# Kernel optimization log

Hardware: AMD Instinct MI355X
Metric: run time of the kernel (lower is better)

The kernel has to match this reference:

```python
import jax, jax.numpy as jnp
import numpy as np

N = 100000   # nodes
E = 3200000  # edges (avg degree 32)
D = 128      # in_channels
H = 128      # hidden_channels
A, S, ETH = 3, 2, 3  # head output dims


def _w(k, o, i):
    return jax.random.normal(k, (o, i), dtype=jnp.float32) / np.sqrt(i).astype(np.float32)


def setup_inputs() -> dict:
    key = jax.random.key(0)
    ks = jax.random.split(key, 20)
    x = jax.random.normal(ks[0], (N, D), dtype=jnp.float32)
    edge_index = jax.random.randint(ks[1], (2, E), 0, N, dtype=jnp.int64)
    inp = {"x": x, "edge_index": edge_index}
    # SAGEConv params: Wl applied to mean-aggregated neighbors, Wr to root, plus bias
    dims = [("1", D, H), ("2", H, H), ("3", H, H), ("a", H, A), ("s", H, S), ("e", H, ETH)]
    ki = 2
    for tag, i, o in dims:
        inp[f"W{tag}l"] = _w(ks[ki], o, i); ki += 1
        inp[f"W{tag}r"] = _w(ks[ki], o, i); ki += 1
        inp[f"b{tag}"] = jnp.zeros((o,), dtype=jnp.float32)
    return inp


def _sage(x, src, dst, inv_deg, Wl, Wr, b):
    # mean aggregation of source features onto destination nodes, then linear
    agg = jax.ops.segment_sum(x[src], dst, num_segments=N) * inv_deg  # [N, d]
    return agg @ Wl.T + x @ Wr.T + b


def reference(x, edge_index,
              W1l, W1r, b1, W2l, W2r, b2, W3l, W3r, b3,
              Wal, War, ba, Wsl, Wsr, bs, Wel, Wer, be):
    src, dst = edge_index[0], edge_index[1]
    deg = jax.ops.segment_sum(jnp.ones((E,), jnp.float32), dst, num_segments=N)
    inv_deg = (1.0 / jnp.maximum(deg, 1.0))[:, None]  # [N,1]
    h = jax.nn.relu(_sage(x, src, dst, inv_deg, W1l, W1r, b1))
    h = jax.nn.relu(_sage(h, src, dst, inv_deg, W2l, W2r, b2))
    h = jax.nn.relu(_sage(h, src, dst, inv_deg, W3l, W3r, b3))
    age_out = _sage(h, src, dst, inv_deg, Wal, War, ba)
    sex_out = _sage(h, src, dst, inv_deg, Wsl, Wsr, bs)
    eth_out = _sage(h, src, dst, inv_deg, Wel, Wer, be)
    return (age_out, sex_out, eth_out)
```

## Files before the change

### kernel.cpp

```cpp
#include <hip/hip_runtime.h>

#define TPB 256
#define NB1 256
#define NBUCK 512

using half4_t = __attribute__((ext_vector_type(4))) _Float16;
using half8_t = __attribute__((ext_vector_type(8))) _Float16;
using f32x4 = __attribute__((ext_vector_type(4))) float;


__global__ __launch_bounds__(256) void hist1_k(const int* __restrict__ ei,
                                               int* __restrict__ hist, int E, int stripe) {
  __shared__ int h[NBUCK];
  for (int i = threadIdx.x; i < NBUCK; i += 256) h[i] = 0;
  __syncthreads();
  int b0 = blockIdx.x * stripe;
  int b1 = min(b0 + stripe, E);
  for (int e = b0 + threadIdx.x; e < b1; e += 256) atomicAdd(&h[ei[E + e] >> 8], 1);
  __syncthreads();
  for (int i = threadIdx.x; i < NBUCK; i += 256) hist[i * NB1 + blockIdx.x] = h[i];
}

__global__ void scan1_k(const int* __restrict__ src, int* __restrict__ out,
                        int* __restrict__ chunk, int n) {
  __shared__ int sh[TPB];
  int i = blockIdx.x * TPB + threadIdx.x;
  int v = (i < n) ? src[i] : 0;
  sh[threadIdx.x] = v;
  __syncthreads();
  for (int off = 1; off < TPB; off <<= 1) {
    int t = (threadIdx.x >= off) ? sh[threadIdx.x - off] : 0;
    __syncthreads();
    sh[threadIdx.x] += t;
    __syncthreads();
  }
  if (i < n) out[i] = sh[threadIdx.x] - v;
  if (threadIdx.x == TPB - 1) chunk[blockIdx.x] = sh[TPB - 1];
}

__global__ void scan2_k(int* __restrict__ chunk, int nb) {
  __shared__ int sh[512];
  int v = (threadIdx.x < nb) ? chunk[threadIdx.x] : 0;
  sh[threadIdx.x] = v;
  __syncthreads();
  for (int off = 1; off < 512; off <<= 1) {
    int t = (threadIdx.x >= off) ? sh[threadIdx.x - off] : 0;
    __syncthreads();
    sh[threadIdx.x] += t;
    __syncthreads();
  }
  if (threadIdx.x < nb) chunk[threadIdx.x] = sh[threadIdx.x] - v;
}

__global__ void scan3_k(int* __restrict__ out, const int* __restrict__ chunk, int n) {
  int i = blockIdx.x * TPB + threadIdx.x;
  if (i < n) out[i] += chunk[blockIdx.x];
}

__global__ __launch_bounds__(256) void scatter1_k(const int* __restrict__ ei,
                                                  const int* __restrict__ base,
                                                  unsigned* __restrict__ ebuf, int E,
                                                  int stripe) {
  __shared__ int cur[NBUCK];
  for (int i = threadIdx.x; i < NBUCK; i += 256) cur[i] = base[i * NB1 + blockIdx.x];
  __syncthreads();
  int b0 = blockIdx.x * stripe;
  int b1 = min(b0 + stripe, E);
  for (int e = b0 + threadIdx.x; e < b1; e += 256) {
    int s = ei[e];
    int d = ei[E + e];
    int p = atomicAdd(&cur[d >> 8], 1);
    ebuf[p] = (unsigned)s | ((unsigned)(d & 255) << 24);
  }
}

__global__ __launch_bounds__(256) void build_k(const unsigned* __restrict__ ebuf,
                                               const int* __restrict__ base,
                                               int* __restrict__ row_start,
                                               int* __restrict__ deg,
                                               float* __restrict__ invd,
                                               int* __restrict__ csr, int N, int E) {
  __shared__ int h[256];
  __shared__ int excl[256];
  __shared__ int bse[2];
  int b = blockIdx.x;
  int t = threadIdx.x;
  if (t == 0) {
    bse[0] = base[b * NB1];
    bse[1] = (b + 1 < NBUCK) ? base[(b + 1) * NB1] : E;
  }
  h[t] = 0;
  __syncthreads();
  int bs = bse[0], be = bse[1];
  for (int e = bs + t; e < be; e += 256) atomicAdd(&h[ebuf[e] >> 24], 1);
  __syncthreads();
  int v = h[t];
  excl[t] = v;
  __syncthreads();
  for (int off = 1; off < 256; off <<= 1) {
    int tv = (t >= off) ? excl[t - off] : 0;
    __syncthreads();
    excl[t] += tv;
    __syncthreads();
  }
  int ex = excl[t] - v;
  int node = b * 256 + t;
  if (node < N) {
    row_start[node] = bs + ex;
    deg[node] = v;
    invd[node] = 1.0f / fmaxf((float)v, 1.0f);
  }
  h[t] = bs + ex;
  __syncthreads();
  for (int e = bs + t; e < be; e += 256) {
    unsigned p = ebuf[e];
    int pos = atomicAdd(&h[p >> 24], 1);
    csr[pos] = (int)(p & 0xFFFFFFu);
  }
}


__global__ void f2h_k(const float* __restrict__ in, _Float16* __restrict__ out, int n4) {
  int i = blockIdx.x * TPB + threadIdx.x;
  if (i < n4) {
    float4 v = ((const float4*)in)[i];
    half4_t o;
    o.x = (_Float16)v.x; o.y = (_Float16)v.y; o.z = (_Float16)v.z; o.w = (_Float16)v.w;
    ((half4_t*)out)[i] = o;
  }
}

__global__ void w6_k(const float* __restrict__ w0, const float* __restrict__ w1,
                     const float* __restrict__ w2, const float* __restrict__ w3,
                     const float* __restrict__ w4, const float* __restrict__ w5,
                     _Float16* __restrict__ out) {
  int t = blockIdx.x * TPB + threadIdx.x;
  if (t >= 6 * 4096) return;
  int which = t >> 12, i = t & 4095;
  const float* src = which == 0 ? w0 : which == 1 ? w1 : which == 2 ? w2
                   : which == 3 ? w3 : which == 4 ? w4 : w5;
  float4 v = ((const float4*)src)[i];
  half4_t o;
  o.x = (_Float16)v.x; o.y = (_Float16)v.y; o.z = (_Float16)v.z; o.w = (_Float16)v.w;
  ((half4_t*)out)[(size_t)which * 4096 + i] = o;
}


__global__ void pack_head_k(const float* __restrict__ Wal, const float* __restrict__ War,
                            const float* __restrict__ ba, const float* __restrict__ Wsl,
                            const float* __restrict__ Wsr, const float* __restrict__ bsx,
                            const float* __restrict__ Wel, const float* __restrict__ Wer,
                            const float* __restrict__ be, _Float16* __restrict__ Wcat,
                            float* __restrict__ bcat) {
  int t = blockIdx.x * TPB + threadIdx.x;
  float v = 0.f;
  bool ok = t < 2048;
  if (t < 384) v = Wal[t];
  else if (t < 640) v = Wsl[t - 384];
  else if (t < 1024) v = Wel[t - 640];
  else if (t < 1408) v = War[t - 1024];
  else if (t < 1664) v = Wsr[t - 1408];
  else if (t < 2048) v = Wer[t - 1664];
  if (ok) Wcat[t] = (_Float16)v;
  if (t < 16) {
    float b = 0.f;
    if (t >= 8 && t < 11) b = ba[t - 8];
    else if (t >= 11 && t < 13) b = bsx[t - 11];
    else if (t >= 13) b = be[t - 13];
    bcat[t] = b;
  }
}


__global__ __launch_bounds__(256) void fused_sage_k(
    const _Float16* __restrict__ hin, const _Float16* __restrict__ Wh,
    const float* __restrict__ bias, const int* __restrict__ csr,
    const int* __restrict__ row_start, const int* __restrict__ deg,
    const float* __restrict__ invd, _Float16* __restrict__ hout,
    const _Float16* __restrict__ Wcat, const float* __restrict__ bcat,
    float* __restrict__ head_out, int n, int mode) {
  __shared__ _Float16 At[16][144];
  int wave = threadIdx.x >> 6;
  int lane = threadIdx.x & 63;
  int g = lane >> 4;
  int l = lane & 15;
  int ms = blockIdx.x * 16;

  const _Float16* gbase = hin + (l << 3);
  int nb = ms + wave * 4;
  int rs[4], dg[4];
#pragma unroll
  for (int i = 0; i < 4; ++i) {
    int nd = nb + i;
    bool ok = nd < n;
    rs[i] = ok ? row_start[nd] : 0;
    dg[i] = ok ? deg[nd] : 0;
  }
  int nid[4];
  if (dg[0] >= 16) {
#pragma unroll
    for (int p = 0; p < 4; ++p) nid[p] = csr[rs[0] + 4 * p + g];
  }
  for (int i = 0; i < 4; ++i) {
    int s = rs[i], c = dg[i];
    float a0 = 0.f, a1 = 0.f, a2 = 0.f, a3 = 0.f;
    float a4 = 0.f, a5 = 0.f, a6 = 0.f, a7 = 0.f;
    int j = 0;
    if (c >= 16) {
      int id[4];
#pragma unroll
      for (int p = 0; p < 4; ++p) id[p] = nid[p];
      while (true) {
        half8_t v[4];
#pragma unroll
        for (int p = 0; p < 4; ++p) v[p] = *(const half8_t*)&gbase[(size_t)id[p] * 128];
        j += 16;
        bool more = (j + 16 <= c);
        if (more) {
#pragma unroll
          for (int p = 0; p < 4; ++p) id[p] = csr[s + j + 4 * p + g];
        }
#pragma unroll
        for (int p = 0; p < 4; ++p) {
          a0 += (float)v[p][0]; a1 += (float)v[p][1];
          a2 += (float)v[p][2]; a3 += (float)v[p][3];
          a4 += (float)v[p][4]; a5 += (float)v[p][5];
          a6 += (float)v[p][6]; a7 += (float)v[p][7];
        }
        if (!more) break;
      }
    }
    if (i < 3 && dg[i + 1] >= 16) {
#pragma unroll
      for (int p = 0; p < 4; ++p) nid[p] = csr[rs[i + 1] + 4 * p + g];
    }
    if (j < c) {
      int cm1 = c - 1;
#pragma unroll
      for (int p = 0; p < 4; ++p) {
        int e = j + 4 * p + g;
        float m = (e < c) ? 1.f : 0.f;
        int id = csr[s + min(e, cm1)];
        half8_t v = *(const half8_t*)&gbase[(size_t)id * 128];
        a0 = fmaf(m, (float)v[0], a0); a1 = fmaf(m, (float)v[1], a1);
        a2 = fmaf(m, (float)v[2], a2); a3 = fmaf(m, (float)v[3], a3);
        a4 = fmaf(m, (float)v[4], a4); a5 = fmaf(m, (float)v[5], a5);
        a6 = fmaf(m, (float)v[6], a6); a7 = fmaf(m, (float)v[7], a7);
      }
    }
    a0 += __shfl_xor(a0, 16); a1 += __shfl_xor(a1, 16);
    a2 += __shfl_xor(a2, 16); a3 += __shfl_xor(a3, 16);
    a4 += __shfl_xor(a4, 16); a5 += __shfl_xor(a5, 16);
    a6 += __shfl_xor(a6, 16); a7 += __shfl_xor(a7, 16);
    a0 += __shfl_xor(a0, 32); a1 += __shfl_xor(a1, 32);
    a2 += __shfl_xor(a2, 32); a3 += __shfl_xor(a3, 32);
    a4 += __shfl_xor(a4, 32); a5 += __shfl_xor(a5, 32);
    a6 += __shfl_xor(a6, 32); a7 += __shfl_xor(a7, 32);
    if (g == 0) {
      int node = nb + i;
      float w = (node < n) ? invd[node] : 0.f;
      half8_t r;
      r[0] = (_Float16)(a0 * w); r[1] = (_Float16)(a1 * w);
      r[2] = (_Float16)(a2 * w); r[3] = (_Float16)(a3 * w);
      r[4] = (_Float16)(a4 * w); r[5] = (_Float16)(a5 * w);
      r[6] = (_Float16)(a6 * w); r[7] = (_Float16)(a7 * w);
      *(half8_t*)&At[wave * 4 + i][l << 3] = r;
    }
  }
  __syncthreads();

  int arow = ms + l;
  bool valid = arow < n;
  f32x4 acc[2];
  acc[0] = (f32x4){0.f, 0.f, 0.f, 0.f};
  acc[1] = (f32x4){0.f, 0.f, 0.f, 0.f};

#pragma unroll
  for (int kb = 0; kb < 128; kb += 32) {
    half8_t af = *(const half8_t*)&At[l][kb + g * 8];
#pragma unroll
    for (int ct = 0; ct < 2; ++ct) {
      int ocol = wave * 32 + ct * 16 + l;
      half8_t bf = *(const half8_t*)&Wh[(size_t)ocol * 128 + kb + g * 8];
      acc[ct] = __builtin_amdgcn_mfma_f32_16x16x32_f16(af, bf, acc[ct], 0, 0, 0);
    }
  }
  {
    const _Float16* W2 = Wh + 16384;
    size_t abase = (size_t)arow * 128 + g * 8;
#pragma unroll
    for (int kb = 0; kb < 128; kb += 32) {
      half8_t af;
      if (valid) {
        af = *(const half8_t*)&hin[abase + kb];
      } else {
#pragma unroll
        for (int jj = 0; jj < 8; ++jj) af[jj] = (_Float16)0;
      }
#pragma unroll
      for (int ct = 0; ct < 2; ++ct) {
        int ocol = wave * 32 + ct * 16 + l;
        half8_t bf = *(const half8_t*)&W2[(size_t)ocol * 128 + kb + g * 8];
        acc[ct] = __builtin_amdgcn_mfma_f32_16x16x32_f16(af, bf, acc[ct], 0, 0, 0);
      }
    }
  }

  if (mode == 0) {
#pragma unroll
    for (int ct = 0; ct < 2; ++ct) {
      int col = wave * 32 + ct * 16 + l;
      float bcol = bias[col];
#pragma unroll
      for (int r = 0; r < 4; ++r) {
        int row = ms + g * 4 + r;
        if (row < n) {
          float v = fmaxf(acc[ct][r] + bcol, 0.f);
          hout[(size_t)row * 128 + col] = (_Float16)v;
        }
      }
    }
  } else {
    __syncthreads();
#pragma unroll
    for (int ct = 0; ct < 2; ++ct) {
      int col = wave * 32 + ct * 16 + l;
      float bcol = bias[col];
#pragma unroll
      for (int r = 0; r < 4; ++r) {
        float v = fmaxf(acc[ct][r] + bcol, 0.f);
        At[g * 4 + r][col] = (_Float16)v;
      }
    }
    __syncthreads();
    if (wave == 0) {
      f32x4 ah = (f32x4){0.f, 0.f, 0.f, 0.f};
#pragma unroll
      for (int kb = 0; kb < 128; kb += 32) {
        half8_t af = *(const half8_t*)&At[l][kb + g * 8];
        half8_t bf = *(const half8_t*)&Wcat[(size_t)l * 128 + kb + g * 8];
        ah = __builtin_amdgcn_mfma_f32_16x16x32_f16(af, bf, ah, 0, 0, 0);
      }
      float bcol = bcat[l];
#pragma unroll
      for (int r = 0; r < 4; ++r) {
        int row = ms + g * 4 + r;
        if (row < n) head_out[(size_t)row * 16 + l] = ah[r] + bcol;
      }
    }
  }
}


__global__ void agg8_k(const float* __restrict__ hlr, const int* __restrict__ csr,
                       const int* __restrict__ row_start, const int* __restrict__ deg,
                       const float* __restrict__ invd, float* __restrict__ out, int n) {
  int node = (blockIdx.x << 2) + (threadIdx.x >> 6);
  if (node >= n) return;
  int lane = threadIdx.x & 63;
  int c2 = lane & 3;
  int g = lane >> 2;
  int s = row_start[node], cnt = deg[node];
  float ax = 0.f, ay = 0.f;
  int j = 0;
  for (; j + 32 <= cnt; j += 32) {
#pragma unroll
    for (int p = 0; p < 2; ++p) {
      int id = csr[s + j + 16 * p + g];
      float2 v = *(const float2*)&hlr[(size_t)id * 16 + 2 * c2];
      ax += v.x;
      ay += v.y;
    }
  }
  if (j < cnt) {
    int cm1 = cnt - 1;
#pragma unroll
    for (int p = 0; p < 2; ++p) {
      int e = j + 16 * p + g;
      float m = (e < cnt) ? 1.f : 0.f;
      int id = csr[s + min(e, cm1)];
      float2 v = *(const float2*)&hlr[(size_t)id * 16 + 2 * c2];
      ax = fmaf(m, v.x, ax);
      ay = fmaf(m, v.y, ay);
    }
  }
  ax += __shfl_xor(ax, 4);  ay += __shfl_xor(ay, 4);
  ax += __shfl_xor(ax, 8);  ay += __shfl_xor(ay, 8);
  ax += __shfl_xor(ax, 16); ay += __shfl_xor(ay, 16);
  ax += __shfl_xor(ax, 32); ay += __shfl_xor(ay, 32);
  if (g == 0) {
    float w = invd[node];
    float r0 = ax * w + hlr[(size_t)node * 16 + 8 + 2 * c2];
    float r1 = ay * w + hlr[(size_t)node * 16 + 8 + 2 * c2 + 1];
    float rr[2] = {r0, r1};
#pragma unroll
    for (int q = 0; q < 2; ++q) {
      int f = 2 * c2 + q;
      float r = rr[q];
      if (f < 3) out[(size_t)node * 3 + f] = r;
      else if (f < 5) out[(size_t)3 * n + (size_t)node * 2 + (f - 3)] = r;
      else out[(size_t)5 * n + (size_t)node * 3 + (f - 5)] = r;
    }
  }
}


extern "C" void kernel_launch(void* const* d_in, const int* in_sizes, int n_in,
                              void* d_out, int out_size, void* d_ws, size_t ws_size,
                              hipStream_t stream) {
  const float* x = (const float*)d_in[0];
  const int* ei = (const int*)d_in[1];
  const float* W1l = (const float*)d_in[2];
  const float* W1r = (const float*)d_in[3];
  const float* b1 = (const float*)d_in[4];
  const float* W2l = (const float*)d_in[5];
  const float* W2r = (const float*)d_in[6];
  const float* b2 = (const float*)d_in[7];
  const float* W3l = (const float*)d_in[8];
  const float* W3r = (const float*)d_in[9];
  const float* b3 = (const float*)d_in[10];
  const float* Wal = (const float*)d_in[11];
  const float* War = (const float*)d_in[12];
  const float* ba = (const float*)d_in[13];
  const float* Wsl = (const float*)d_in[14];
  const float* Wsr = (const float*)d_in[15];
  const float* bsx = (const float*)d_in[16];
  const float* Wel = (const float*)d_in[17];
  const float* Wer = (const float*)d_in[18];
  const float* be = (const float*)d_in[19];

  int N = in_sizes[0] / 128;
  int E = in_sizes[1] / 2;
  int NBKT = (N + 255) >> 8;

  char* w = (char*)d_ws;
  auto alloc = [&](size_t b) {
    char* p = w;
    w += (b + 255) & ~(size_t)255;
    return p;
  };
  int* deg = (int*)alloc((size_t)N * 4);
  int* row_start = (int*)alloc((size_t)N * 4);
  float* invd = (float*)alloc((size_t)N * 4);
  int* hist = (int*)alloc((size_t)NBUCK * NB1 * 4);
  int* chunk = (int*)alloc(512 * 4);
  int* csr = (int*)alloc((size_t)E * 4);
  size_t xh_bytes = (size_t)N * 128 * 2;
  size_t ebuf_bytes = (size_t)E * 4;
  char* region = (char*)alloc(xh_bytes > ebuf_bytes ? xh_bytes : ebuf_bytes);
  unsigned* ebuf = (unsigned*)region;
  _Float16* xh = (_Float16*)region;
  _Float16* hA = (_Float16*)alloc((size_t)N * 128 * 2);
  _Float16* hB = (_Float16*)alloc((size_t)N * 128 * 2);
  _Float16* wh = (_Float16*)alloc((size_t)6 * 16384 * 2);
  _Float16* Wcat = (_Float16*)alloc(2048 * 2);
  float* bcat = (float*)alloc(16 * 4);
  float* head_lr = (float*)alloc((size_t)N * 16 * 4);

  int stripe = (((E + NB1 - 1) / NB1) + 255) & ~255;
  int nscan = NBUCK * NB1;
  int nbScan = (nscan + TPB - 1) / TPB;
  int nbNode = (N + 3) / 4;
  int nbM = (N + 15) / 16;
  int nbC = (N * 32 + TPB - 1) / TPB;

  hist1_k<<<NB1, 256, 0, stream>>>(ei, hist, E, stripe);
  scan1_k<<<nbScan, TPB, 0, stream>>>(hist, hist, chunk, nscan);
  scan2_k<<<1, 512, 0, stream>>>(chunk, nbScan);
  scan3_k<<<nbScan, TPB, 0, stream>>>(hist, chunk, nscan);
  scatter1_k<<<NB1, 256, 0, stream>>>(ei, hist, ebuf, E, stripe);
  build_k<<<NBKT, 256, 0, stream>>>(ebuf, hist, row_start, deg, invd, csr, N, E);

  f2h_k<<<nbC, TPB, 0, stream>>>(x, xh, N * 32);
  w6_k<<<96, TPB, 0, stream>>>(W1l, W1r, W2l, W2r, W3l, W3r, wh);
  pack_head_k<<<8, TPB, 0, stream>>>(Wal, War, ba, Wsl, Wsr, bsx, Wel, Wer, be, Wcat, bcat);

  fused_sage_k<<<nbM, TPB, 0, stream>>>(xh, wh + 0 * 16384, b1, csr, row_start, deg,
                                        invd, hA, nullptr, nullptr, nullptr, N, 0);
  fused_sage_k<<<nbM, TPB, 0, stream>>>(hA, wh + 2 * 16384, b2, csr, row_start, deg,
                                        invd, hB, nullptr, nullptr, nullptr, N, 0);
  fused_sage_k<<<nbM, TPB, 0, stream>>>(hB, wh + 4 * 16384, b3, csr, row_start, deg,
                                        invd, nullptr, Wcat, bcat, head_lr, N, 1);
  agg8_k<<<nbNode, TPB, 0, stream>>>(head_lr, csr, row_start, deg, invd, (float*)d_out, N);
}
```

Measured before the change: 688.4 us.

## Make fused SAGE layer wave-independent, removing block-wide barriers

Each wave now owns its own 4-node tile and private LDS buffers, then computes all 128 output columns with MFMA using only 4 of the 16 A rows (replicated via l&3). This drops every __syncthreads, so waves no longer wait on the slowest gather in the block. Outputs are staged in LDS so hout is written as coalesced half8 rows, and the head GEMM runs per wave. In exchange, each wave does four times the MFMA work and weight loads per node, since 12 of the 16 rows are redundant.

```diff
diff --git a/kernel.cpp b/kernel.cpp
--- a/kernel.cpp
+++ b/kernel.cpp
@@ -179,19 +179,23 @@
     const float* __restrict__ invd, _Float16* __restrict__ hout,
     const _Float16* __restrict__ Wcat, const float* __restrict__ bcat,
     float* __restrict__ head_out, int n, int mode) {
-  __shared__ _Float16 At[16][144];
+  __shared__ _Float16 At[4][4][144];
+  __shared__ _Float16 Ot4[4][4][144];
   int wave = threadIdx.x >> 6;
   int lane = threadIdx.x & 63;
   int g = lane >> 4;
   int l = lane & 15;
-  int ms = blockIdx.x * 16;
+  _Float16(*A)[144] = At[wave];
+  _Float16(*Ot)[144] = Ot4[wave];
+
+  int tb = (blockIdx.x * 4 + wave) * 4;
+  if (tb >= n) return;
 
   const _Float16* gbase = hin + (l << 3);
-  int nb = ms + wave * 4;
   int rs[4], dg[4];
 #pragma unroll
   for (int i = 0; i < 4; ++i) {
-    int nd = nb + i;
+    int nd = tb + i;
     bool ok = nd < n;
     rs[i] = ok ? row_start[nd] : 0;
     dg[i] = ok ? deg[nd] : 0;
@@ -257,95 +261,84 @@
     a4 += __shfl_xor(a4, 32); a5 += __shfl_xor(a5, 32);
     a6 += __shfl_xor(a6, 32); a7 += __shfl_xor(a7, 32);
     if (g == 0) {
-      int node = nb + i;
+      int node = tb + i;
       float w = (node < n) ? invd[node] : 0.f;
       half8_t r;
       r[0] = (_Float16)(a0 * w); r[1] = (_Float16)(a1 * w);
       r[2] = (_Float16)(a2 * w); r[3] = (_Float16)(a3 * w);
       r[4] = (_Float16)(a4 * w); r[5] = (_Float16)(a5 * w);
       r[6] = (_Float16)(a6 * w); r[7] = (_Float16)(a7 * w);
-      *(half8_t*)&At[wave * 4 + i][l << 3] = r;
-    }
-  }
-  __syncthreads();
-
-  int arow = ms + l;
-  bool valid = arow < n;
-  f32x4 acc[2];
-  acc[0] = (f32x4){0.f, 0.f, 0.f, 0.f};
-  acc[1] = (f32x4){0.f, 0.f, 0.f, 0.f};
-
-#pragma unroll
-  for (int kb = 0; kb < 128; kb += 32) {
-    half8_t af = *(const half8_t*)&At[l][kb + g * 8];
-#pragma unroll
-    for (int ct = 0; ct < 2; ++ct) {
-      int ocol = wave * 32 + ct * 16 + l;
-      half8_t bf = *(const half8_t*)&Wh[(size_t)ocol * 128 + kb + g * 8];
-      acc[ct] = __builtin_amdgcn_mfma_f32_16x16x32_f16(af, bf, acc[ct], 0, 0, 0);
-    }
-  }
-  {
-    const _Float16* W2 = Wh + 16384;
-    size_t abase = (size_t)arow * 128 + g * 8;
+      *(half8_t*)&A[i][l << 3] = r;
+    }
+  }
+
+  const _Float16* W2 = Wh + 16384;
+  int rrow = tb + (l & 3);
+  bool rv = rrow < n;
+  size_t rbase = (size_t)rrow * 128 + g * 8;
+#pragma unroll
+  for (int ch = 0; ch < 2; ++ch) {
+    f32x4 acc[4];
+#pragma unroll
+    for (int ct = 0; ct < 4; ++ct) acc[ct] = (f32x4){0.f, 0.f, 0.f, 0.f};
+#pragma unroll
+    for (int kb = 0; kb < 128; kb += 32) {
+      half8_t af = *(const half8_t*)&A[l & 3][kb + g * 8];
+#pragma unroll
+      for (int ct = 0; ct < 4; ++ct) {
+        int col = ch * 64 + ct * 16 + l;
+        half8_t bf = *(const half8_t*)&Wh[(size_t)col * 128 + kb + g * 8];
+        acc[ct] = __builtin_amdgcn_mfma_f32_16x16x32_f16(af, bf, acc[ct], 0, 0, 0);
+      }
+    }
 #pragma unroll
     for (int kb = 0; kb < 128; kb += 32) {
       half8_t af;
-      if (valid) {
-        af = *(const half8_t*)&hin[abase + kb];
+      if (rv) {
+        af = *(const half8_t*)&hin[rbase + kb];
       } else {
 #pragma unroll
         for (int jj = 0; jj < 8; ++jj) af[jj] = (_Float16)0;
       }
 #pragma unroll
-      for (int ct = 0; ct < 2; ++ct) {
-        int ocol = wave * 32 + ct * 16 + l;
-        half8_t bf = *(const half8_t*)&W2[(size_t)ocol * 128 + kb + g * 8];
+      for (int ct = 0; ct < 4; ++ct) {
+        int col = ch * 64 + ct * 16 + l;
+        half8_t bf = *(const half8_t*)&W2[(size_t)col * 128 + kb + g * 8];
         acc[ct] = __builtin_amdgcn_mfma_f32_16x16x32_f16(af, bf, acc[ct], 0, 0, 0);
       }
     }
+    if (g == 0) {
+#pragma unroll
+      for (int ct = 0; ct < 4; ++ct) {
+        int col = ch * 64 + ct * 16 + l;
+        float bc = bias[col];
+#pragma unroll
+        for (int r = 0; r < 4; ++r) {
+          Ot[r][col] = (_Float16)fmaxf(acc[ct][r] + bc, 0.f);
+        }
+      }
+    }
   }
 
   if (mode == 0) {
-#pragma unroll
-    for (int ct = 0; ct < 2; ++ct) {
-      int col = wave * 32 + ct * 16 + l;
-      float bcol = bias[col];
+    int rr = lane >> 4, j = lane & 15;
+    int orow = tb + rr;
+    if (orow < n)
+      *(half8_t*)&hout[(size_t)orow * 128 + j * 8] = *(const half8_t*)&Ot[rr][j * 8];
+  } else {
+    f32x4 ah = (f32x4){0.f, 0.f, 0.f, 0.f};
+#pragma unroll
+    for (int kb = 0; kb < 128; kb += 32) {
+      half8_t af = *(const half8_t*)&Ot[l & 3][kb + g * 8];
+      half8_t bf = *(const half8_t*)&Wcat[(size_t)l * 128 + kb + g * 8];
+      ah = __builtin_amdgcn_mfma_f32_16x16x32_f16(af, bf, ah, 0, 0, 0);
+    }
+    if (g == 0) {
+      float bc = bcat[l];
 #pragma unroll
       for (int r = 0; r < 4; ++r) {
-        int row = ms + g * 4 + r;
-        if (row < n) {
-          float v = fmaxf(acc[ct][r] + bcol, 0.f);
-          hout[(size_t)row * 128 + col] = (_Float16)v;
-        }
-      }
-    }
-  } else {
-    __syncthreads();
-#pragma unroll
-    for (int ct = 0; ct < 2; ++ct) {
-      int col = wave * 32 + ct * 16 + l;
-      float bcol = bias[col];
-#pragma unroll
-      for (int r = 0; r < 4; ++r) {
-        float v = fmaxf(acc[ct][r] + bcol, 0.f);
-        At[g * 4 + r][col] = (_Float16)v;
-      }
-    }
-    __syncthreads();
-    if (wave == 0) {
-      f32x4 ah = (f32x4){0.f, 0.f, 0.f, 0.f};
-#pragma unroll
-      for (int kb = 0; kb < 128; kb += 32) {
-        half8_t af = *(const half8_t*)&At[l][kb + g * 8];
-        half8_t bf = *(const half8_t*)&Wcat[(size_t)l * 128 + kb + g * 8];
-        ah = __builtin_amdgcn_mfma_f32_16x16x32_f16(af, bf, ah, 0, 0, 0);
-      }
-      float bcol = bcat[l];
-#pragma unroll
-      for (int r = 0; r < 4; ++r) {
-        int row = ms + g * 4 + r;
-        if (row < n) head_out[(size_t)row * 16 + l] = ah[r] + bcol;
+        int orow = tb + r;
+        if (orow < n) head_out[(size_t)orow * 16 + l] = ah[r] + bc;
       }
     }
   }
```

Result: slower. 1.123 ms (+63.2%).

## Use persistent atomic tile scheduling, merge prep kernels, split head buffers

Applied to the files above, without the earlier changes.

The three SAGE layer kernels now run a fixed grid of 2048 persistent blocks. Each block pulls 16-node tiles from a global atomic counter until none remain, instead of launching one block per tile. This aims to balance degree-dependent work and cut block-launch overhead, at the cost of one atomic and one barrier per tile. The three small conversion and packing kernels are merged into one prep kernel that also zeroes the tile counters, saving launches. The head output is split into separate 8-wide gather and root buffers, so the final aggregation gathers denser 32-byte rows.

```diff
diff --git a/kernel.cpp b/kernel.cpp
--- a/kernel.cpp
+++ b/kernel.cpp
@@ -120,48 +120,43 @@
 }
 
 
-__global__ void f2h_k(const float* __restrict__ in, _Float16* __restrict__ out, int n4) {
-  int i = blockIdx.x * TPB + threadIdx.x;
-  if (i < n4) {
-    float4 v = ((const float4*)in)[i];
+__global__ void prep_k(const float* __restrict__ x, _Float16* __restrict__ xh, int n4,
+                       const float* __restrict__ w0, const float* __restrict__ w1,
+                       const float* __restrict__ w2, const float* __restrict__ w3,
+                       const float* __restrict__ w4, const float* __restrict__ w5,
+                       _Float16* __restrict__ wh,
+                       const float* __restrict__ Wal, const float* __restrict__ War,
+                       const float* __restrict__ ba, const float* __restrict__ Wsl,
+                       const float* __restrict__ Wsr, const float* __restrict__ bsx,
+                       const float* __restrict__ Wel, const float* __restrict__ Wer,
+                       const float* __restrict__ be, _Float16* __restrict__ Wcat,
+                       float* __restrict__ bcat, int* __restrict__ ctrs) {
+  int t = blockIdx.x * TPB + threadIdx.x;
+  if (t < n4) {
+    float4 v = ((const float4*)x)[t];
     half4_t o;
     o.x = (_Float16)v.x; o.y = (_Float16)v.y; o.z = (_Float16)v.z; o.w = (_Float16)v.w;
-    ((half4_t*)out)[i] = o;
-  }
-}
-
-__global__ void w6_k(const float* __restrict__ w0, const float* __restrict__ w1,
-                     const float* __restrict__ w2, const float* __restrict__ w3,
-                     const float* __restrict__ w4, const float* __restrict__ w5,
-                     _Float16* __restrict__ out) {
-  int t = blockIdx.x * TPB + threadIdx.x;
-  if (t >= 6 * 4096) return;
-  int which = t >> 12, i = t & 4095;
-  const float* src = which == 0 ? w0 : which == 1 ? w1 : which == 2 ? w2
-                   : which == 3 ? w3 : which == 4 ? w4 : w5;
-  float4 v = ((const float4*)src)[i];
-  half4_t o;
-  o.x = (_Float16)v.x; o.y = (_Float16)v.y; o.z = (_Float16)v.z; o.w = (_Float16)v.w;
-  ((half4_t*)out)[(size_t)which * 4096 + i] = o;
-}
-
-
-__global__ void pack_head_k(const float* __restrict__ Wal, const float* __restrict__ War,
-                            const float* __restrict__ ba, const float* __restrict__ Wsl,
-                            const float* __restrict__ Wsr, const float* __restrict__ bsx,
-                            const float* __restrict__ Wel, const float* __restrict__ Wer,
-                            const float* __restrict__ be, _Float16* __restrict__ Wcat,
-                            float* __restrict__ bcat) {
-  int t = blockIdx.x * TPB + threadIdx.x;
-  float v = 0.f;
-  bool ok = t < 2048;
-  if (t < 384) v = Wal[t];
-  else if (t < 640) v = Wsl[t - 384];
-  else if (t < 1024) v = Wel[t - 640];
-  else if (t < 1408) v = War[t - 1024];
-  else if (t < 1664) v = Wsr[t - 1408];
-  else if (t < 2048) v = Wer[t - 1664];
-  if (ok) Wcat[t] = (_Float16)v;
+    ((half4_t*)xh)[t] = o;
+  }
+  if (t < 6 * 4096) {
+    int which = t >> 12, i = t & 4095;
+    const float* src = which == 0 ? w0 : which == 1 ? w1 : which == 2 ? w2
+                     : which == 3 ? w3 : which == 4 ? w4 : w5;
+    float4 v = ((const float4*)src)[i];
+    half4_t o;
+    o.x = (_Float16)v.x; o.y = (_Float16)v.y; o.z = (_Float16)v.z; o.w = (_Float16)v.w;
+    ((half4_t*)wh)[(size_t)which * 4096 + i] = o;
+  }
+  if (t < 2048) {
+    float v = 0.f;
+    if (t < 384) v = Wal[t];
+    else if (t < 640) v = Wsl[t - 384];
+    else if (t < 1024) v = Wel[t - 640];
+    else if (t < 1408) v = War[t - 1024];
+    else if (t < 1664) v = Wsr[t - 1408];
+    else v = Wer[t - 1664];
+    Wcat[t] = (_Float16)v;
+  }
   if (t < 16) {
     float b = 0.f;
     if (t >= 8 && t < 11) b = ba[t - 8];
@@ -169,6 +164,7 @@
     else if (t >= 13) b = be[t - 13];
     bcat[t] = b;
   }
+  if (t < 4) ctrs[t] = 0;
 }
 
 
@@ -178,183 +174,197 @@
     const int* __restrict__ row_start, const int* __restrict__ deg,
     const float* __restrict__ invd, _Float16* __restrict__ hout,
     const _Float16* __restrict__ Wcat, const float* __restrict__ bcat,
-    float* __restrict__ head_out, int n, int mode) {
+    float* __restrict__ head_g, float* __restrict__ head_r,
+    int* __restrict__ ctr, int ntiles, int n, int mode) {
   __shared__ _Float16 At[16][144];
+  __shared__ int tile_s;
   int wave = threadIdx.x >> 6;
   int lane = threadIdx.x & 63;
   int g = lane >> 4;
   int l = lane & 15;
-  int ms = blockIdx.x * 16;
-
   const _Float16* gbase = hin + (l << 3);
-  int nb = ms + wave * 4;
-  int rs[4], dg[4];
-#pragma unroll
-  for (int i = 0; i < 4; ++i) {
-    int nd = nb + i;
-    bool ok = nd < n;
-    rs[i] = ok ? row_start[nd] : 0;
-    dg[i] = ok ? deg[nd] : 0;
-  }
-  int nid[4];
-  if (dg[0] >= 16) {
-#pragma unroll
-    for (int p = 0; p < 4; ++p) nid[p] = csr[rs[0] + 4 * p + g];
-  }
-  for (int i = 0; i < 4; ++i) {
-    int s = rs[i], c = dg[i];
-    float a0 = 0.f, a1 = 0.f, a2 = 0.f, a3 = 0.f;
-    float a4 = 0.f, a5 = 0.f, a6 = 0.f, a7 = 0.f;
-    int j = 0;
-    if (c >= 16) {
-      int id[4];
-#pragma unroll
-      for (int p = 0; p < 4; ++p) id[p] = nid[p];
-      while (true) {
-        half8_t v[4];
-#pragma unroll
-        for (int p = 0; p < 4; ++p) v[p] = *(const half8_t*)&gbase[(size_t)id[p] * 128];
-        j += 16;
-        bool more = (j + 16 <= c);
-        if (more) {
-#pragma unroll
-          for (int p = 0; p < 4; ++p) id[p] = csr[s + j + 4 * p + g];
-        }
+  const _Float16* W2 = Wh + 16384;
+
+  for (;;) {
+    if (threadIdx.x == 0) tile_s = atomicAdd(ctr, 1);
+    __syncthreads();
+    int tile = tile_s;
+    if (tile >= ntiles) break;
+    int ms = tile * 16;
+
+    int nb = ms + wave * 4;
+    int rs[4], dg[4];
+#pragma unroll
+    for (int i = 0; i < 4; ++i) {
+      int nd = nb + i;
+      bool ok = nd < n;
+      rs[i] = ok ? row_start[nd] : 0;
+      dg[i] = ok ? deg[nd] : 0;
+    }
+    int nid[4];
+    if (dg[0] >= 16) {
+#pragma unroll
+      for (int p = 0; p < 4; ++p) nid[p] = csr[rs[0] + 4 * p + g];
+    }
+    for (int i = 0; i < 4; ++i) {
+      int s = rs[i], c = dg[i];
+      float a0 = 0.f, a1 = 0.f, a2 = 0.f, a3 = 0.f;
+      float a4 = 0.f, a5 = 0.f, a6 = 0.f, a7 = 0.f;
+      int j = 0;
+      if (c >= 16) {
+        int id[4];
+#pragma unroll
+        for (int p = 0; p < 4; ++p) id[p] = nid[p];
+        while (true) {
+          half8_t v[4];
+#pragma unroll
+          for (int p = 0; p < 4; ++p) v[p] = *(const half8_t*)&gbase[(size_t)id[p] * 128];
+          j += 16;
+          bool more = (j + 16 <= c);
+          if (more) {
+#pragma unroll
+            for (int p = 0; p < 4; ++p) id[p] = csr[s + j + 4 * p + g];
+          }
+#pragma unroll
+          for (int p = 0; p < 4; ++p) {
+            a0 += (float)v[p][0]; a1 += (float)v[p][1];
+            a2 += (float)v[p][2]; a3 += (float)v[p][3];
+            a4 += (float)v[p][4]; a5 += (float)v[p][5];
+            a6 += (float)v[p][6]; a7 += (float)v[p][7];
+          }
+          if (!more) break;
+        }
+      }
+      if (i < 3 && dg[i + 1] >= 16) {
+#pragma unroll
+        for (int p = 0; p < 4; ++p) nid[p] = csr[rs[i + 1] + 4 * p + g];
+      }
+      if (j < c) {
+        int cm1 = c - 1;
 #pragma unroll
         for (int p = 0; p < 4; ++p) {
-          a0 += (float)v[p][0]; a1 += (float)v[p][1];
-          a2 += (float)v[p][2]; a3 += (float)v[p][3];
-          a4 += (float)v[p][4]; a5 += (float)v[p][5];
-          a6 += (float)v[p][6]; a7 += (float)v[p][7];
-        }
-        if (!more) break;
-      }
-    }
-    if (i < 3 && dg[i + 1] >= 16) {
-#pragma unroll
-      for (int p = 0; p < 4; ++p) nid[p] = csr[rs[i + 1] + 4 * p + g];
-    }
-    if (j < c) {
-      int cm1 = c - 1;
-#pragma unroll
-      for (int p = 0; p < 4; ++p) {
-        int e = j + 4 * p + g;
-        float m = (e < c) ? 1.f : 0.f;
-        int id = csr[s + min(e, cm1)];
-        half8_t v = *(const half8_t*)&gbase[(size_t)id * 128];
-        a0 = fmaf(m, (float)v[0], a0); a1 = fmaf(m, (float)v[1], a1);
-        a2 = fmaf(m, (float)v[2], a2); a3 = fmaf(m, (float)v[3], a3);
-        a4 = fmaf(m, (float)v[4], a4); a5 = fmaf(m, (float)v[5], a5);
-        a6 = fmaf(m, (float)v[6], a6); a7 = fmaf(m, (float)v[7], a7);
-      }
-    }
-    a0 += __shfl_xor(a0, 16); a1 += __shfl_xor(a1, 16);
-    a2 += __shfl_xor(a2, 16); a3 += __shfl_xor(a3, 16);
-    a4 += __shfl_xor(a4, 16); a5 += __shfl_xor(a5, 16);
-    a6 += __shfl_xor(a6, 16); a7 += __shfl_xor(a7, 16);
-    a0 += __shfl_xor(a0, 32); a1 += __shfl_xor(a1, 32);
-    a2 += __shfl_xor(a2, 32); a3 += __shfl_xor(a3, 32);
-    a4 += __shfl_xor(a4, 32); a5 += __shfl_xor(a5, 32);
-    a6 += __shfl_xor(a6, 32); a7 += __shfl_xor(a7, 32);
-    if (g == 0) {
-      int node = nb + i;
-      float w = (node < n) ? invd[node] : 0.f;
-      half8_t r;
-      r[0] = (_Float16)(a0 * w); r[1] = (_Float16)(a1 * w);
-      r[2] = (_Float16)(a2 * w); r[3] = (_Float16)(a3 * w);
-      r[4] = (_Float16)(a4 * w); r[5] = (_Float16)(a5 * w);
-      r[6] = (_Float16)(a6 * w); r[7] = (_Float16)(a7 * w);
-      *(half8_t*)&At[wave * 4 + i][l << 3] = r;
-    }
-  }
-  __syncthreads();
-
-  int arow = ms + l;
-  bool valid = arow < n;
-  f32x4 acc[2];
-  acc[0] = (f32x4){0.f, 0.f, 0.f, 0.f};
-  acc[1] = (f32x4){0.f, 0.f, 0.f, 0.f};
-
-#pragma unroll
-  for (int kb = 0; kb < 128; kb += 32) {
-    half8_t af = *(const half8_t*)&At[l][kb + g * 8];
-#pragma unroll
-    for (int ct = 0; ct < 2; ++ct) {
-      int ocol = wave * 32 + ct * 16 + l;
-      half8_t bf = *(const half8_t*)&Wh[(size_t)ocol * 128 + kb + g * 8];
-      acc[ct] = __builtin_amdgcn_mfma_f32_16x16x32_f16(af, bf, acc[ct], 0, 0, 0);
-    }
-  }
-  {
-    const _Float16* W2 = Wh + 16384;
-    size_t abase = (size_t)arow * 128 + g * 8;
+          int e = j + 4 * p + g;
+          float m = (e < c) ? 1.f : 0.f;
+          int id = csr[s + min(e, cm1)];
+          half8_t v = *(const half8_t*)&gbase[(size_t)id * 128];
+          a0 = fmaf(m, (float)v[0], a0); a1 = fmaf(m, (float)v[1], a1);
+          a2 = fmaf(m, (float)v[2], a2); a3 = fmaf(m, (float)v[3], a3);
+          a4 = fmaf(m, (float)v[4], a4); a5 = fmaf(m, (float)v[5], a5);
+          a6 = fmaf(m, (float)v[6], a6); a7 = fmaf(m, (float)v[7], a7);
+        }
+      }
+      a0 += __shfl_xor(a0, 16); a1 += __shfl_xor(a1, 16);
+      a2 += __shfl_xor(a2, 16); a3 += __shfl_xor(a3, 16);
+      a4 += __shfl_xor(a4, 16); a5 += __shfl_xor(a5, 16);
+      a6 += __shfl_xor(a6, 16); a7 += __shfl_xor(a7, 16);
+      a0 += __shfl_xor(a0, 32); a1 += __shfl_xor(a1, 32);
+      a2 += __shfl_xor(a2, 32); a3 += __shfl_xor(a3, 32);
+      a4 += __shfl_xor(a4, 32); a5 += __shfl_xor(a5, 32);
+      a6 += __shfl_xor(a6, 32); a7 += __shfl_xor(a7, 32);
+      if (g == 0) {
+        int node = nb + i;
+        float w = (node < n) ? invd[node] : 0.f;
+        half8_t r;
+        r[0] = (_Float16)(a0 * w); r[1] = (_Float16)(a1 * w);
+        r[2] = (_Float16)(a2 * w); r[3] = (_Float16)(a3 * w);
+        r[4] = (_Float16)(a4 * w); r[5] = (_Float16)(a5 * w);
+        r[6] = (_Float16)(a6 * w); r[7] = (_Float16)(a7 * w);
+        *(half8_t*)&At[wave * 4 + i][l << 3] = r;
+      }
+    }
+    __syncthreads();
+
+    int arow = ms + l;
+    bool valid = arow < n;
+    f32x4 acc[2];
+    acc[0] = (f32x4){0.f, 0.f, 0.f, 0.f};
+    acc[1] = (f32x4){0.f, 0.f, 0.f, 0.f};
+
 #pragma unroll
     for (int kb = 0; kb < 128; kb += 32) {
-      half8_t af;
-      if (valid) {
-        af = *(const half8_t*)&hin[abase + kb];
-      } else {
-#pragma unroll
-        for (int jj = 0; jj < 8; ++jj) af[jj] = (_Float16)0;
-      }
+      half8_t af = *(const half8_t*)&At[l][kb + g * 8];
 #pragma unroll
       for (int ct = 0; ct < 2; ++ct) {
         int ocol = wave * 32 + ct * 16 + l;
-        half8_t bf = *(const half8_t*)&W2[(size_t)ocol * 128 + kb + g * 8];
+        half8_t bf = *(const half8_t*)&Wh[(size_t)ocol * 128 + kb + g * 8];
         acc[ct] = __builtin_amdgcn_mfma_f32_16x16x32_f16(af, bf, acc[ct], 0, 0, 0);
       }
     }
-  }
-
-  if (mode == 0) {
-#pragma unroll
-    for (int ct = 0; ct < 2; ++ct) {
-      int col = wave * 32 + ct * 16 + l;
-      float bcol = bias[col];
-#pragma unroll
-      for (int r = 0; r < 4; ++r) {
-        int row = ms + g * 4 + r;
-        if (row < n) {
+    {
+      size_t abase = (size_t)arow * 128 + g * 8;
+#pragma unroll
+      for (int kb = 0; kb < 128; kb += 32) {
+        half8_t af;
+        if (valid) {
+          af = *(const half8_t*)&hin[abase + kb];
+        } else {
+#pragma unroll
+          for (int jj = 0; jj < 8; ++jj) af[jj] = (_Float16)0;
+        }
+#pragma unroll
+        for (int ct = 0; ct < 2; ++ct) {
+          int ocol = wave * 32 + ct * 16 + l;
+          half8_t bf = *(const half8_t*)&W2[(size_t)ocol * 128 + kb + g * 8];
+          acc[ct] = __builtin_amdgcn_mfma_f32_16x16x32_f16(af, bf, acc[ct], 0, 0, 0);
+        }
+      }
+    }
+
+    if (mode == 0) {
+#pragma unroll
+      for (int ct = 0; ct < 2; ++ct) {
+        int col = wave * 32 + ct * 16 + l;
+        float bcol = bias[col];
+#pragma unroll
+        for (int r = 0; r < 4; ++r) {
+          int row = ms + g * 4 + r;
+          if (row < n) {
+            float v = fmaxf(acc[ct][r] + bcol, 0.f);
+            hout[(size_t)row * 128 + col] = (_Float16)v;
+          }
+        }
+      }
+    } else {
+      __syncthreads();
+#pragma unroll
+      for (int ct = 0; ct < 2; ++ct) {
+        int col = wave * 32 + ct * 16 + l;
+        float bcol = bias[col];
+#pragma unroll
+        for (int r = 0; r < 4; ++r) {
           float v = fmaxf(acc[ct][r] + bcol, 0.f);
-          hout[(size_t)row * 128 + col] = (_Float16)v;
-        }
-      }
-    }
-  } else {
-    __syncthreads();
-#pragma unroll
-    for (int ct = 0; ct < 2; ++ct) {
-      int col = wave * 32 + ct * 16 + l;
-      float bcol = bias[col];
-#pragma unroll
-      for (int r = 0; r < 4; ++r) {
-        float v = fmaxf(acc[ct][r] + bcol, 0.f);
-        At[g * 4 + r][col] = (_Float16)v;
-      }
-    }
-    __syncthreads();
-    if (wave == 0) {
-      f32x4 ah = (f32x4){0.f, 0.f, 0.f, 0.f};
-#pragma unroll
-      for (int kb = 0; kb < 128; kb += 32) {
-        half8_t af = *(const half8_t*)&At[l][kb + g * 8];
-        half8_t bf = *(const half8_t*)&Wcat[(size_t)l * 128 + kb + g * 8];
-        ah = __builtin_amdgcn_mfma_f32_16x16x32_f16(af, bf, ah, 0, 0, 0);
-      }
-      float bcol = bcat[l];
-#pragma unroll
-      for (int r = 0; r < 4; ++r) {
-        int row = ms + g * 4 + r;
-        if (row < n) head_out[(size_t)row * 16 + l] = ah[r] + bcol;
-      }
-    }
-  }
-}
-
-
-__global__ void agg8_k(const float* __restrict__ hlr, const int* __restrict__ csr,
-                       const int* __restrict__ row_start, const int* __restrict__ deg,
-                       const float* __restrict__ invd, float* __restrict__ out, int n) {
+          At[g * 4 + r][col] = (_Float16)v;
+        }
+      }
+      __syncthreads();
+      if (wave == 0) {
+        f32x4 ah = (f32x4){0.f, 0.f, 0.f, 0.f};
+#pragma unroll
+        for (int kb = 0; kb < 128; kb += 32) {
+          half8_t af = *(const half8_t*)&At[l][kb + g * 8];
+          half8_t bf = *(const half8_t*)&Wcat[(size_t)l * 128 + kb + g * 8];
+          ah = __builtin_amdgcn_mfma_f32_16x16x32_f16(af, bf, ah, 0, 0, 0);
+        }
+        float bc = bcat[l];
+#pragma unroll
+        for (int r = 0; r < 4; ++r) {
+          int orow = ms + g * 4 + r;
+          if (orow < n) {
+            float v = ah[r] + bc;
+            if (l < 8) head_g[(size_t)orow * 8 + l] = v;
+            else head_r[(size_t)orow * 8 + (l - 8)] = v;
+          }
+        }
+      }
+    }
+  }
+}
+
+
+__global__ void agg8_k(const float* __restrict__ head_g, const float* __restrict__ head_r,
+                       const int* __restrict__ csr, const int* __restrict__ row_start,
+                       const int* __restrict__ deg, const float* __restrict__ invd,
+                       float* __restrict__ out, int n) {
   int node = (blockIdx.x << 2) + (threadIdx.x >> 6);
   if (node >= n) return;
   int lane = threadIdx.x & 63;
@@ -367,7 +377,7 @@
 #pragma unroll
     for (int p = 0; p < 2; ++p) {
       int id = csr[s + j + 16 * p + g];
-      float2 v = *(const float2*)&hlr[(size_t)id * 16 + 2 * c2];
+      float2 v = *(const float2*)&head_g[(size_t)id * 8 + 2 * c2];
       ax += v.x;
       ay += v.y;
     }
@@ -379,7 +389,7 @@
       int e = j + 16 * p + g;
       float m = (e < cnt) ? 1.f : 0.f;
       int id = csr[s + min(e, cm1)];
-      float2 v = *(const float2*)&hlr[(size_t)id * 16 + 2 * c2];
+      float2 v = *(const float2*)&head_g[(size_t)id * 8 + 2 * c2];
       ax = fmaf(m, v.x, ax);
       ay = fmaf(m, v.y, ay);
     }
@@ -390,8 +400,8 @@
   ax += __shfl_xor(ax, 32); ay += __shfl_xor(ay, 32);
   if (g == 0) {
     float w = invd[node];
-    float r0 = ax * w + hlr[(size_t)node * 16 + 8 + 2 * c2];
-    float r1 = ay * w + hlr[(size_t)node * 16 + 8 + 2 * c2 + 1];
+    float r0 = ax * w + head_r[(size_t)node * 8 + 2 * c2];
+    float r1 = ay * w + head_r[(size_t)node * 8 + 2 * c2 + 1];
     float rr[2] = {r0, r1};
 #pragma unroll
     for (int q = 0; q < 2; ++q) {
@@ -455,14 +465,17 @@
   _Float16* wh = (_Float16*)alloc((size_t)6 * 16384 * 2);
   _Float16* Wcat = (_Float16*)alloc(2048 * 2);
   float* bcat = (float*)alloc(16 * 4);
-  float* head_lr = (float*)alloc((size_t)N * 16 * 4);
+  float* head_g = (float*)alloc((size_t)N * 8 * 4);
+  float* head_r = (float*)alloc((size_t)N * 8 * 4);
+  int* ctrs = (int*)alloc(4 * 4);
 
   int stripe = (((E + NB1 - 1) / NB1) + 255) & ~255;
   int nscan = NBUCK * NB1;
   int nbScan = (nscan + TPB - 1) / TPB;
   int nbNode = (N + 3) / 4;
-  int nbM = (N + 15) / 16;
+  int ntiles = (N + 15) / 16;
   int nbC = (N * 32 + TPB - 1) / TPB;
+  int PGRID = 2048;
 
   hist1_k<<<NB1, 256, 0, stream>>>(ei, hist, E, stripe);
   scan1_k<<<nbScan, TPB, 0, stream>>>(hist, hist, chunk, nscan);
@@ -471,15 +484,19 @@
   scatter1_k<<<NB1, 256, 0, stream>>>(ei, hist, ebuf, E, stripe);
   build_k<<<NBKT, 256, 0, stream>>>(ebuf, hist, row_start, deg, invd, csr, N, E);
 
-  f2h_k<<<nbC, TPB, 0, stream>>>(x, xh, N * 32);
-  w6_k<<<96, TPB, 0, stream>>>(W1l, W1r, W2l, W2r, W3l, W3r, wh);
-  pack_head_k<<<8, TPB, 0, stream>>>(Wal, War, ba, Wsl, Wsr, bsx, Wel, Wer, be, Wcat, bcat);
-
-  fused_sage_k<<<nbM, TPB, 0, stream>>>(xh, wh + 0 * 16384, b1, csr, row_start, deg,
-                                        invd, hA, nullptr, nullptr, nullptr, N, 0);
-  fused_sage_k<<<nbM, TPB, 0, stream>>>(hA, wh + 2 * 16384, b2, csr, row_start, deg,
-                                        invd, hB, nullptr, nullptr, nullptr, N, 0);
-  fused_sage_k<<<nbM, TPB, 0, stream>>>(hB, wh + 4 * 16384, b3, csr, row_start, deg,
-                                        invd, nullptr, Wcat, bcat, head_lr, N, 1);
-  agg8_k<<<nbNode, TPB, 0, stream>>>(head_lr, csr, row_start, deg, invd, (float*)d_out, N);
-}
+  prep_k<<<nbC, TPB, 0, stream>>>(x, xh, N * 32, W1l, W1r, W2l, W2r, W3l, W3r, wh,
+                                  Wal, War, ba, Wsl, Wsr, bsx, Wel, Wer, be, Wcat,
+                                  bcat, ctrs);
+
+  fused_sage_k<<<PGRID, TPB, 0, stream>>>(xh, wh + 0 * 16384, b1, csr, row_start, deg,
+                                          invd, hA, nullptr, nullptr, nullptr, nullptr,
+                                          ctrs + 0, ntiles, N, 0);
+  fused_sage_k<<<PGRID, TPB, 0, stream>>>(hA, wh + 2 * 16384, b2, csr, row_start, deg,
+                                          invd, hB, nullptr, nullptr, nullptr, nullptr,
+                                          ctrs + 1, ntiles, N, 0);
+  fused_sage_k<<<PGRID, TPB, 0, stream>>>(hB, wh + 4 * 16384, b3, csr, row_start, deg,
+                                          invd, nullptr, Wcat, bcat, head_g, head_r,
+                                          ctrs + 2, ntiles, N, 1);
+  agg8_k<<<nbNode, TPB, 0, stream>>>(head_g, head_r, csr, row_start, deg, invd,
+                                     (float*)d_out, N);
+}
```

After: 767.1 us. 11.4% more time.
